# Kernel optimization log

Hardware: AMD Instinct MI355X
Metric: run time of the kernel (lower is better)

## Reference

```python
import jax, jax.numpy as jnp
import numpy as np

B, S, D = 2, 400, 512  # batch, seq (src == tgt for self-attention), dim; attn_hidden=0 so d == D


def setup_inputs() -> dict:
    key = jax.random.key(0)
    ks = jax.random.split(key, 9)
    inv = 1.0 / np.sqrt(D)
    return {
        "input": jax.random.normal(ks[0], (B, S, D), jnp.float32),
        "memory_bank": jax.random.normal(ks[1], (B, S, D), jnp.float32),
        # lengths in [S//2, S], guaranteed >= 2 so no row is fully masked
        "memory_lengths": jax.random.randint(ks[2], (B,), S // 2, S + 1, jnp.int32),
        "Wq": jax.random.normal(ks[3], (D, D), jnp.float32) * inv,   # linear_query.weight^T
        "bq": jax.random.normal(ks[4], (D,), jnp.float32) * inv,      # linear_query.bias
        "Wc": jax.random.normal(ks[5], (D, D), jnp.float32) * inv,   # linear_context.weight^T
        "v": jax.random.normal(ks[6], (D,), jnp.float32) * inv,       # v.weight (d -> 1)
        "Wout": jax.random.normal(ks[7], (2 * D, D), jnp.float32) * inv,  # linear_out.weight^T
        "bout": jax.random.normal(ks[8], (D,), jnp.float32) * inv,
    }


def reference(input, memory_bank, memory_lengths, Wq, bq, Wc, v, Wout, bout):
    b, s, d = memory_bank.shape
    # Bahdanau/mlp score: v^T tanh(Wq q + b + Wc h)
    wq = jnp.einsum("btd,de->bte", input, Wq) + bq            # [B,T,d]
    uh = jnp.einsum("bsd,de->bse", memory_bank, Wc)           # [B,S,d]
    wquh = jnp.tanh(wq[:, :, None, :] + uh[:, None, :, :])    # [B,T,S,d] big intermediate
    scores = jnp.einsum("btse,e->bts", wquh, v)               # [B,T,S]
    # padding mask (j < length) with self position masked out on the diagonal
    pos = jnp.arange(s)
    key_mask = pos[None, :] < memory_lengths[:, None]         # [B,S]
    mask = key_mask[:, None, :] & (pos[:, None] != pos[None, :])  # [B,T,S]
    scores = jnp.where(mask, scores, -jnp.inf)
    align = jax.nn.softmax(scores, axis=2)                    # [B,T,S]
    c = jnp.einsum("bts,bsd->btd", align, memory_bank)        # context [B,T,D]
    concat_c = jnp.concatenate([c, input], axis=2)            # [B,T,2D]
    attn_h = jnp.einsum("btf,fd->btd", concat_c, Wout) + bout # [B,T,D]
    # mlp variant: no sigmoid gating
    return attn_h.transpose(1, 0, 2), align.transpose(1, 0, 2)  # [T,B,D], [T,B,S]
```

## Files before the change

### kernel.cpp

```cpp
#include <hip/hip_runtime.h>
#include <math.h>

#define BB 2
#define SS 400
#define DD 512
#define TWO_LOG2E 2.8853900817779268f

#if __has_builtin(__builtin_amdgcn_exp2f)
#define EXP2F(x) __builtin_amdgcn_exp2f(x)
#else
#define EXP2F(x) exp2f(x)
#endif
#define RCPF(x) __builtin_amdgcn_rcpf(x)

#define EAOFF 0
#define MOFF 409600
#define EB4OFF 819200
#define XOFF 1228800

typedef __bf16 bf16x8 __attribute__((ext_vector_type(8)));
typedef float floatx16 __attribute__((ext_vector_type(16)));

__global__ __launch_bounds__(256) void k0_all(
    const float* __restrict__ Wq, const float* __restrict__ Wc,
    const float* __restrict__ Wout, const float* __restrict__ input,
    const float* __restrict__ mbk, unsigned short* __restrict__ wt,
    unsigned short* __restrict__ ahi, unsigned short* __restrict__ alo)
{
    const int gid = blockIdx.x;
    if (gid < 1024) {
        const int g   = gid >> 9;
        const int rem = gid & 511;
        const int k0  = (rem & 15) * 32;
        const int n0  = (rem >> 4) * 32;

        __shared__ float tile[32][33];
        const int nn  = threadIdx.x & 31;
        const int kk0 = threadIdx.x >> 5;
        const int n   = n0 + nn;

        #pragma unroll
        for (int p = 0; p < 4; ++p) {
            const int k = k0 + kk0 + p * 8;
            float val;
            if (n0 < 512) val = (g ? Wc : Wq)[(size_t)k * 512 + n];
            else          val = Wout[((size_t)(g ? k : 512 + k)) * 512 + (n - 512)];
            tile[kk0 + p * 8][nn] = val;
        }
        __syncthreads();

        const int kc = threadIdx.x & 31;
        #pragma unroll
        for (int p = 0; p < 4; ++p) {
            const int nl = (threadIdx.x >> 5) + p * 8;
            const __bf16 h = (__bf16)tile[kc][nl];
            wt[((size_t)(g * 1024 + n0 + nl)) * 512 + k0 + kc] =
                __builtin_bit_cast(unsigned short, h);
        }
    } else {
        const int cid = gid - 1024;
        const int g   = (cid >= 400) ? 1 : 0;
        const int i4  = (cid - g * 400) * 256 + threadIdx.x;
        const float4 a = ((const float4*)(g ? mbk : input))[i4];
        ushort4 h, l;
        #pragma unroll
        for (int j = 0; j < 4; ++j) {
            const float av = (&a.x)[j];
            const __bf16 hh = (__bf16)av;
            (&h.x)[j] = __builtin_bit_cast(unsigned short, hh);
            const __bf16 ll = (__bf16)(av - (float)hh);
            (&l.x)[j] = __builtin_bit_cast(unsigned short, ll);
        }
        ((ushort4*)(ahi + (size_t)g * 409600))[i4] = h;
        ((ushort4*)(alo + (size_t)g * 409600))[i4] = l;
    }
}

__global__ __launch_bounds__(64) void k1_mfma(
    const unsigned short* __restrict__ ahi, const unsigned short* __restrict__ alo,
    const unsigned short* __restrict__ wt, const float* __restrict__ bq,
    const float* __restrict__ bout, float* __restrict__ ws,
    float* __restrict__ out0)
{
    const int lane = threadIdx.x;
    const int mt   = blockIdx.x;
    const int np   = blockIdx.y;
    const int g    = blockIdx.z;
    const int m    = lane & 31;
    const int kh   = lane >> 5;
    const int n0   = np * 64;

    const size_t arow = ((size_t)g * 800 + mt * 32 + m) * 512 + kh * 8;
    const unsigned short* __restrict__ ah = ahi + arow;
    const unsigned short* __restrict__ al = alo + arow;
    const unsigned short* __restrict__ w0 =
        wt + ((size_t)(g * 1024 + n0 + m)) * 512 + kh * 8;
    const unsigned short* __restrict__ w1 = w0 + (size_t)32 * 512;

    floatx16 acc0h, acc0l, acc1h, acc1l;
    #pragma unroll
    for (int i = 0; i < 16; ++i) { acc0h[i] = 0.f; acc0l[i] = 0.f;
                                   acc1h[i] = 0.f; acc1l[i] = 0.f; }

    #pragma unroll 4
    for (int ks = 0; ks < 32; ++ks) {
        const bf16x8 va0 = *(const bf16x8*)(ah + ks * 16);
        const bf16x8 va1 = *(const bf16x8*)(al + ks * 16);
        const bf16x8 bh0 = *(const bf16x8*)(w0 + ks * 16);
        const bf16x8 bh1 = *(const bf16x8*)(w1 + ks * 16);

        acc0h = __builtin_amdgcn_mfma_f32_32x32x16_bf16(va0, bh0, acc0h, 0, 0, 0);
        acc0l = __builtin_amdgcn_mfma_f32_32x32x16_bf16(va1, bh0, acc0l, 0, 0, 0);
        acc1h = __builtin_amdgcn_mfma_f32_32x32x16_bf16(va0, bh1, acc1h, 0, 0, 0);
        acc1l = __builtin_amdgcn_mfma_f32_32x32x16_bf16(va1, bh1, acc1l, 0, 0, 0);
    }

    const floatx16 c0 = acc0h + acc0l;
    const floatx16 c1 = acc1h + acc1l;
    const int rbase = kh * 4;

    #pragma unroll
    for (int r = 0; r < 16; ++r) {
        const int row  = (r & 3) + 8 * (r >> 2) + rbase;
        const int grow = mt * 32 + row;
        const int bi   = (grow >= SS) ? 1 : 0;
        const int rl   = grow - bi * SS;
        #pragma unroll
        for (int u = 0; u < 2; ++u) {
            const float val  = u ? c1[r] : c0[r];
            const int   gcol = n0 + u * 32 + m;
            if (g == 0) {
                if (gcol < 512) {
                    ws[EAOFF + (size_t)grow * 512 + gcol] =
                        EXP2F(TWO_LOG2E * (val + bq[gcol]));
                } else {
                    const int d = gcol - 512;
                    out0[((size_t)(rl * BB + bi)) * 512 + d] = val + bout[d];
                }
            } else {
                if (gcol < 512) {
                    ws[EB4OFF + (size_t)((bi * 128 + (gcol >> 2)) * SS + rl) * 4
                       + (gcol & 3)] = EXP2F(TWO_LOG2E * val);
                } else {
                    ws[MOFF + (size_t)grow * 512 + (gcol - 512)] = val;
                }
            }
        }
    }
}

__global__ __launch_bounds__(512) void k2_attn(
    const float* __restrict__ ws, const float* __restrict__ v,
    const int* __restrict__ lens, float* __restrict__ out1,
    float* __restrict__ out0)
{
    const int tq = blockIdx.x;
    const int b  = blockIdx.y;
    const int t0 = tq * 4;
    const int tid = threadIdx.x;
    const int s   = tid;
    const int sidx = (s < SS) ? s : 0;
    const int len  = lens[b];

    __shared__ float lea[4][512];
    __shared__ float lv[512];
    __shared__ float4 lal4[SS];
    __shared__ float wredm[4][8], wreds[4][8];

    lv[tid] = v[tid];
    #pragma unroll
    for (int j = 0; j < 4; ++j)
        lea[j][tid] = ws[EAOFF + (size_t)(b * SS + t0 + j) * 512 + tid];
    __syncthreads();

    const float4* __restrict__ eb4 =
        (const float4*)(ws + EB4OFF) + (size_t)b * 128 * SS + sidx;

    float acc[4] = {0.f, 0.f, 0.f, 0.f};
    #pragma unroll 4
    for (int e4 = 0; e4 < 128; ++e4) {
        const float4 eb = eb4[(size_t)e4 * SS];
        const float4 vv = *(const float4*)&lv[e4 * 4];
        #pragma unroll
        for (int j = 0; j < 4; ++j) {
            const float4 ea = *(const float4*)&lea[j][e4 * 4];
            const float d0 = fmaf(ea.x, eb.x, 1.f);
            const float d1 = fmaf(ea.y, eb.y, 1.f);
            const float d2 = fmaf(ea.z, eb.z, 1.f);
            const float d3 = fmaf(ea.w, eb.w, 1.f);
            const float d01 = d0 * d1, d23 = d2 * d3;
            const float n01 = fmaf(vv.x, d1, vv.y * d0);
            const float n23 = fmaf(vv.z, d3, vv.w * d2);
            const float num = fmaf(n01, d23, n23 * d01);
            acc[j] = fmaf(num, RCPF(d01 * d23), acc[j]);
        }
    }

    const int wid  = tid >> 6;
    const int lane = tid & 63;

    bool  ok[4];
    float sc[4];
    #pragma unroll
    for (int j = 0; j < 4; ++j) {
        ok[j] = (s < SS) && (s < len) && (s != t0 + j);
        sc[j] = ok[j] ? -2.f * acc[j] : -INFINITY;
    }

    float m[4] = {sc[0], sc[1], sc[2], sc[3]};
    #pragma unroll
    for (int off = 32; off > 0; off >>= 1) {
        #pragma unroll
        for (int j = 0; j < 4; ++j)
            m[j] = fmaxf(m[j], __shfl_xor(m[j], off));
    }
    if (lane == 0) {
        #pragma unroll
        for (int j = 0; j < 4; ++j) wredm[j][wid] = m[j];
    }
    __syncthreads();
    float mx[4];
    #pragma unroll
    for (int j = 0; j < 4; ++j) {
        mx[j] = wredm[j][0];
        #pragma unroll
        for (int w = 1; w < 8; ++w) mx[j] = fmaxf(mx[j], wredm[j][w]);
    }
    __syncthreads();

    float p[4];
    #pragma unroll
    for (int j = 0; j < 4; ++j)
        p[j] = ok[j] ? __expf(sc[j] - mx[j]) : 0.f;
    float sv[4] = {p[0], p[1], p[2], p[3]};
    #pragma unroll
    for (int off = 32; off > 0; off >>= 1) {
        #pragma unroll
        for (int j = 0; j < 4; ++j)
            sv[j] += __shfl_xor(sv[j], off);
    }
    if (lane == 0) {
        #pragma unroll
        for (int j = 0; j < 4; ++j) wreds[j][wid] = sv[j];
    }
    __syncthreads();
    float inv[4];
    #pragma unroll
    for (int j = 0; j < 4; ++j) {
        float tot = wreds[j][0];
        #pragma unroll
        for (int w = 1; w < 8; ++w) tot += wreds[j][w];
        inv[j] = RCPF(tot);
    }

    if (s < SS) {
        float4 al;
        al.x = p[0] * inv[0];
        al.y = p[1] * inv[1];
        al.z = p[2] * inv[2];
        al.w = p[3] * inv[3];
        out1[((size_t)((t0 + 0) * BB) + b) * SS + s] = al.x;
        out1[((size_t)((t0 + 1) * BB) + b) * SS + s] = al.y;
        out1[((size_t)((t0 + 2) * BB) + b) * SS + s] = al.z;
        out1[((size_t)((t0 + 3) * BB) + b) * SS + s] = al.w;
        lal4[s] = al;
    }
    __syncthreads();

    const float* __restrict__ Mb = ws + MOFF + (size_t)b * SS * DD;
    const int d = tid;
    float c0 = 0.f, c1 = 0.f, c2 = 0.f, c3 = 0.f;
    #pragma unroll 8
    for (int sp = 0; sp < SS; ++sp) {
        const float  mv = Mb[(size_t)sp * DD + d];
        const float4 la = lal4[sp];
        c0 = fmaf(la.x, mv, c0);
        c1 = fmaf(la.y, mv, c1);
        c2 = fmaf(la.z, mv, c2);
        c3 = fmaf(la.w, mv, c3);
    }
    out0[((size_t)((t0 + 0) * BB) + b) * DD + d] += c0;
    out0[((size_t)((t0 + 1) * BB) + b) * DD + d] += c1;
    out0[((size_t)((t0 + 2) * BB) + b) * DD + d] += c2;
    out0[((size_t)((t0 + 3) * BB) + b) * DD + d] += c3;
}

extern "C" void kernel_launch(void* const* d_in, const int* in_sizes, int n_in,
                              void* d_out, int out_size, void* d_ws, size_t ws_size,
                              hipStream_t stream)
{
    const float* input = (const float*)d_in[0];
    const float* mbk   = (const float*)d_in[1];
    const int*   lens  = (const int*)d_in[2];
    const float* Wq    = (const float*)d_in[3];
    const float* bq    = (const float*)d_in[4];
    const float* Wc    = (const float*)d_in[5];
    const float* v     = (const float*)d_in[6];
    const float* Wout  = (const float*)d_in[7];
    const float* bout  = (const float*)d_in[8];

    float* out0 = (float*)d_out;
    float* out1 = out0 + (size_t)BB * SS * DD;
    float* ws   = (float*)d_ws;
    unsigned short* x16 = (unsigned short*)(ws + XOFF);
    unsigned short* wt  = x16;
    unsigned short* ahi = x16 + 1048576;
    unsigned short* alo = ahi + 819200;

    hipLaunchKernelGGL(k0_all, dim3(1824), dim3(256), 0, stream,
                       Wq, Wc, Wout, input, mbk, wt, ahi, alo);
    hipLaunchKernelGGL(k1_mfma, dim3(25, 16, 2), dim3(64), 0, stream,
                       ahi, alo, wt, bq, bout, ws, out0);
    hipLaunchKernelGGL(k2_attn, dim3(100, 2), dim3(512), 0, stream,
                       ws, v, lens, out1, out0);
}
```

Before: 156.5 us.

## Split attention score kernel over feature halves into separate launch

Splits the fused score+softmax+context kernel in two. The first kernel computes partial tanh-sum scores over half of the feature dimension each (grid doubled to 400 blocks), writing partials to workspace. The second sums the two partials, does softmax and the context reduction. It reads ea and v directly from global instead of LDS. This aims to raise occupancy on the many-CU GPU, at the cost of an extra launch and a partial-score round trip through memory. The context loop unroll is also raised from 8 to 16.

```diff
diff --git a/kernel.cpp b/kernel.cpp
--- a/kernel.cpp
+++ b/kernel.cpp
@@ -17,6 +17,7 @@
 #define MOFF 409600
 #define EB4OFF 819200
 #define XOFF 1228800
+#define SPOFF 2572288
 
 typedef __bf16 bf16x8 __attribute__((ext_vector_type(8)));
 typedef float floatx16 __attribute__((ext_vector_type(16)));
@@ -149,8 +150,62 @@
     }
 }
 
-__global__ __launch_bounds__(512) void k2_attn(
+__global__ __launch_bounds__(512) void k2a_score(
     const float* __restrict__ ws, const float* __restrict__ v,
+    float* __restrict__ sp)
+{
+    const int tq = blockIdx.x;
+    const int b  = blockIdx.y;
+    const int eh = blockIdx.z;
+    const int t0 = tq * 4;
+    const int tid = threadIdx.x;
+    const int s   = tid;
+    const int sidx = (s < SS) ? s : 0;
+
+    const float* __restrict__ ea0p = ws + EAOFF + (size_t)(b * SS + t0) * 512;
+    const float* __restrict__ ea1p = ea0p + 512;
+    const float* __restrict__ ea2p = ea0p + 1024;
+    const float* __restrict__ ea3p = ea0p + 1536;
+    const float4* __restrict__ eb4 =
+        (const float4*)(ws + EB4OFF) + (size_t)b * 128 * SS + sidx;
+
+    float acc0 = 0.f, acc1 = 0.f, acc2 = 0.f, acc3 = 0.f;
+    const int e4b = eh * 64;
+
+#define QUAD(EAP, ACC)                                               \
+    {                                                                \
+        const float4 ea = *(const float4*)(EAP + e4 * 4);            \
+        const float d0 = fmaf(ea.x, eb.x, 1.f);                      \
+        const float d1 = fmaf(ea.y, eb.y, 1.f);                      \
+        const float d2 = fmaf(ea.z, eb.z, 1.f);                      \
+        const float d3 = fmaf(ea.w, eb.w, 1.f);                      \
+        const float d01 = d0 * d1, d23 = d2 * d3;                    \
+        const float n01 = fmaf(vv.x, d1, vv.y * d0);                 \
+        const float n23 = fmaf(vv.z, d3, vv.w * d2);                 \
+        const float num = fmaf(n01, d23, n23 * d01);                 \
+        ACC = fmaf(num, RCPF(d01 * d23), ACC);                       \
+    }
+
+    #pragma unroll 4
+    for (int e4 = e4b; e4 < e4b + 64; ++e4) {
+        const float4 eb = eb4[(size_t)e4 * SS];
+        const float4 vv = *(const float4*)(v + e4 * 4);
+        QUAD(ea0p, acc0)
+        QUAD(ea1p, acc1)
+        QUAD(ea2p, acc2)
+        QUAD(ea3p, acc3)
+    }
+#undef QUAD
+
+    const size_t base = ((size_t)(eh * 2 + b)) * 400;
+    sp[(base + t0 + 0) * 512 + s] = acc0;
+    sp[(base + t0 + 1) * 512 + s] = acc1;
+    sp[(base + t0 + 2) * 512 + s] = acc2;
+    sp[(base + t0 + 3) * 512 + s] = acc3;
+}
+
+__global__ __launch_bounds__(512) void k2b_sm(
+    const float* __restrict__ ws, const float* __restrict__ sp,
     const int* __restrict__ lens, float* __restrict__ out1,
     float* __restrict__ out0)
 {
@@ -159,42 +214,17 @@
     const int t0 = tq * 4;
     const int tid = threadIdx.x;
     const int s   = tid;
-    const int sidx = (s < SS) ? s : 0;
     const int len  = lens[b];
 
-    __shared__ float lea[4][512];
-    __shared__ float lv[512];
     __shared__ float4 lal4[SS];
     __shared__ float wredm[4][8], wreds[4][8];
 
-    lv[tid] = v[tid];
+    const size_t b0 = ((size_t)(0 * 2 + b)) * 400;
+    const size_t b1 = ((size_t)(1 * 2 + b)) * 400;
+    float acc[4];
     #pragma unroll
     for (int j = 0; j < 4; ++j)
-        lea[j][tid] = ws[EAOFF + (size_t)(b * SS + t0 + j) * 512 + tid];
-    __syncthreads();
-
-    const float4* __restrict__ eb4 =
-        (const float4*)(ws + EB4OFF) + (size_t)b * 128 * SS + sidx;
-
-    float acc[4] = {0.f, 0.f, 0.f, 0.f};
-    #pragma unroll 4
-    for (int e4 = 0; e4 < 128; ++e4) {
-        const float4 eb = eb4[(size_t)e4 * SS];
-        const float4 vv = *(const float4*)&lv[e4 * 4];
-        #pragma unroll
-        for (int j = 0; j < 4; ++j) {
-            const float4 ea = *(const float4*)&lea[j][e4 * 4];
-            const float d0 = fmaf(ea.x, eb.x, 1.f);
-            const float d1 = fmaf(ea.y, eb.y, 1.f);
-            const float d2 = fmaf(ea.z, eb.z, 1.f);
-            const float d3 = fmaf(ea.w, eb.w, 1.f);
-            const float d01 = d0 * d1, d23 = d2 * d3;
-            const float n01 = fmaf(vv.x, d1, vv.y * d0);
-            const float n23 = fmaf(vv.z, d3, vv.w * d2);
-            const float num = fmaf(n01, d23, n23 * d01);
-            acc[j] = fmaf(num, RCPF(d01 * d23), acc[j]);
-        }
-    }
+        acc[j] = sp[(b0 + t0 + j) * 512 + s] + sp[(b1 + t0 + j) * 512 + s];
 
     const int wid  = tid >> 6;
     const int lane = tid & 63;
@@ -270,10 +300,10 @@
     const float* __restrict__ Mb = ws + MOFF + (size_t)b * SS * DD;
     const int d = tid;
     float c0 = 0.f, c1 = 0.f, c2 = 0.f, c3 = 0.f;
-    #pragma unroll 8
-    for (int sp = 0; sp < SS; ++sp) {
-        const float  mv = Mb[(size_t)sp * DD + d];
-        const float4 la = lal4[sp];
+    #pragma unroll 16
+    for (int sp2 = 0; sp2 < SS; ++sp2) {
+        const float  mv = Mb[(size_t)sp2 * DD + d];
+        const float4 la = lal4[sp2];
         c0 = fmaf(la.x, mv, c0);
         c1 = fmaf(la.y, mv, c1);
         c2 = fmaf(la.z, mv, c2);
@@ -306,11 +336,14 @@
     unsigned short* wt  = x16;
     unsigned short* ahi = x16 + 1048576;
     unsigned short* alo = ahi + 819200;
+    float* sp = ws + SPOFF;
 
     hipLaunchKernelGGL(k0_all, dim3(1824), dim3(256), 0, stream,
                        Wq, Wc, Wout, input, mbk, wt, ahi, alo);
     hipLaunchKernelGGL(k1_mfma, dim3(25, 16, 2), dim3(64), 0, stream,
                        ahi, alo, wt, bq, bout, ws, out0);
-    hipLaunchKernelGGL(k2_attn, dim3(100, 2), dim3(512), 0, stream,
-                       ws, v, lens, out1, out0);
-}
+    hipLaunchKernelGGL(k2a_score, dim3(100, 2, 2), dim3(512), 0, stream,
+                       ws, v, sp);
+    hipLaunchKernelGGL(k2b_sm, dim3(100, 2), dim3(512), 0, stream,
+                       ws, sp, lens, out1, out0);
+}
```

Result: faster. 140.3 us (median of 2 runs) (-10.3%).
